# Optimization experiments

Measured on AMD Instinct MI355X. Metric: run time of the kernel, lower is better.

Reference implementation:

```python
import jax, jax.numpy as jnp
import numpy as np

N_NODES = 100000
N_EDGES = 1600000
HID = 128


def setup_inputs() -> dict:
    key = jax.random.key(0)
    ks = jax.random.split(key, 16)

    def w(k, fan_in, fan_out, scale=None):
        s = scale if scale is not None else 1.0 / np.sqrt(fan_in)
        return (jax.random.normal(k, (fan_in, fan_out), jnp.float32) * s)

    inp = {
        "h": jax.random.normal(ks[0], (N_NODES, HID), jnp.float32),
        "edge_index": jax.random.randint(ks[1], (2, N_EDGES), 0, N_NODES, jnp.int64),
        "x": jax.random.normal(ks[2], (N_NODES, 3), jnp.float32),
        "v": jax.random.normal(ks[3], (N_NODES, 3), jnp.float32),
        # edge_mlp: Linear(257,128) -> ReLU -> Linear(128,128) -> ReLU
        "we1": w(ks[4], 2 * HID + 1, HID), "be1": jnp.zeros((HID,), jnp.float32),
        "we2": w(ks[5], HID, HID), "be2": jnp.zeros((HID,), jnp.float32),
        # node_mlp: Linear(384,128) -> ReLU -> Linear(128,128)
        "wn1": w(ks[6], 3 * HID, HID), "bn1": jnp.zeros((HID,), jnp.float32),
        "wn2": w(ks[7], HID, HID), "bn2": jnp.zeros((HID,), jnp.float32),
        # coord_mlp_vel: Linear(128,128) -> ReLU -> Linear(128,1)
        "wv1": w(ks[8], HID, HID), "bv1": jnp.zeros((HID,), jnp.float32),
        "wv2": w(ks[9], HID, 1), "bv2": jnp.zeros((1,), jnp.float32),
        # coord_mlp: Linear(128,128) -> ReLU -> Linear(128,1, bias=False, xavier gain 0.001)
        "wc1": w(ks[10], HID, HID), "bc1": jnp.zeros((HID,), jnp.float32),
        "wc2": w(ks[11], HID, 1, scale=0.001),
    }
    return inp


def reference(h, edge_index, x, v, we1, be1, we2, be2, wn1, bn1, wn2, bn2,
              wv1, bv1, wv2, bv2, wc1, bc1, wc2):
    n = h.shape[0]
    row, col = edge_index[0], edge_index[1]

    # coord2radial
    coord_diff = x[row] - x[col]                                  # [M, 3]
    radial = jnp.sum(coord_diff * coord_diff, axis=1, keepdims=True)  # [M, 1]

    # edge_model (no attention, no edge_attr)
    e_in = jnp.concatenate([h[row], h[col], radial], axis=1)      # [M, 257]
    edge_feat = jax.nn.relu(jax.nn.relu(e_in @ we1 + be1) @ we2 + be2)  # [M, 128]

    # coord_model: per-edge scalar gate, clamp, segment-mean over row
    gate = jax.nn.relu(edge_feat @ wc1 + bc1) @ wc2               # [M, 1]
    trans = jnp.clip(coord_diff * gate, -100.0, 100.0)            # [M, 3]
    num = jax.ops.segment_sum(trans, row, num_segments=n)         # [N, 3]
    cnt = jax.ops.segment_sum(jnp.ones_like(trans), row, num_segments=n)
    f = (num / jnp.maximum(cnt, 1.0)) * 1.0                       # coords_weight = 1.0

    # update: v' = gate(h) * v + f ; x' = x + v'
    vel_gate = jax.nn.relu(h @ wv1 + bv1) @ wv2 + bv2             # [N, 1]
    v_new = vel_gate * v + f
    x_new = x + v_new

    # node_model with others=h: cat[h, h, segment_sum(edge_feat)]
    agg = jax.ops.segment_sum(edge_feat, row, num_segments=n)     # [N, 128]
    n_in = jnp.concatenate([h, h, agg], axis=1)                   # [N, 384]
    h_new = h + (jax.nn.relu(n_in @ wn1 + bn1) @ wn2 + bn2)       # recurrent residual

    return h_new, x_new, v_new
```

## Files before the change

### kernel.cpp

```cpp
#include <hip/hip_runtime.h>
#include <hip/hip_bf16.h>
#include <stdint.h>

typedef __bf16 bf16_t;
typedef __bf16 bf16x8 __attribute__((ext_vector_type(8)));
typedef float f32x4 __attribute__((ext_vector_type(4)));

#define HID 128

__device__ __forceinline__ bf16_t* swz(bf16_t* base, int row, int rowBytes, int byteInRow) {
    return (bf16_t*)((char*)base + row * rowBytes + (byteInRow ^ ((row & 7) << 4)));
}
__device__ __forceinline__ const bf16_t* swzc(const bf16_t* base, int row, int rowBytes, int byteInRow) {
    return (const bf16_t*)((const char*)base + row * rowBytes + (byteInRow ^ ((row & 7) << 4)));
}

__device__ __forceinline__ bf16x8 pack8(float4 a, float4 b) {
    bf16x8 r;
    r[0] = (bf16_t)a.x; r[1] = (bf16_t)a.y; r[2] = (bf16_t)a.z; r[3] = (bf16_t)a.w;
    r[4] = (bf16_t)b.x; r[5] = (bf16_t)b.y; r[6] = (bf16_t)b.z; r[7] = (bf16_t)b.w;
    return r;
}

__device__ __forceinline__ bool is_i64(const int* ei) {
    return ((ei[1] | ei[3] | ei[5] | ei[7]) == 0);
}
__device__ __forceinline__ int eidx(const int* __restrict__ ei, int i, bool i64) {
    return i64 ? ei[2 * i] : ei[i];
}

__global__ void prep_kernel(const float* __restrict__ we1, const float* __restrict__ we2,
                            const float* __restrict__ wc1, const float* __restrict__ wn1,
                            const float* __restrict__ wn2, const float* __restrict__ wv1,
                            bf16_t* w1t, float* w1last, bf16_t* w2t, bf16_t* wc1t,
                            bf16_t* wn1t, bf16_t* wn2t, bf16_t* wv1t) {
    int idx = blockIdx.x * 256 + threadIdx.x;
    if (idx < 32768) { int j = idx >> 8, k = idx & 255; w1t[idx] = (bf16_t)we1[k * 128 + j]; return; }
    idx -= 32768;
    if (idx < 128) { w1last[idx] = we1[256 * 128 + idx]; return; }
    idx -= 128;
    if (idx < 16384) { int j = idx >> 7, k = idx & 127; w2t[idx] = (bf16_t)we2[k * 128 + j]; return; }
    idx -= 16384;
    if (idx < 16384) { int j = idx >> 7, k = idx & 127; wc1t[idx] = (bf16_t)wc1[k * 128 + j]; return; }
    idx -= 16384;
    if (idx < 32768) {
        int j = idx >> 8, k = idx & 255;
        float val = (k < 128) ? (wn1[k * 128 + j] + wn1[(k + 128) * 128 + j])
                              : wn1[(k + 128) * 128 + j];
        wn1t[idx] = (bf16_t)val; return;
    }
    idx -= 32768;
    if (idx < 16384) { int j = idx >> 7, k = idx & 127; wn2t[idx] = (bf16_t)wn2[k * 128 + j]; return; }
    idx -= 16384;
    if (idx < 16384) { int j = idx >> 7, k = idx & 127; wv1t[idx] = (bf16_t)wv1[k * 128 + j]; return; }
}

__global__ __launch_bounds__(512, 2) void edge_kernel(
    const float* __restrict__ h, const int* __restrict__ ei, const float* __restrict__ x,
    const float* __restrict__ be1, const float* __restrict__ be2,
    const float* __restrict__ bc1, const float* __restrict__ wc2,
    const bf16_t* __restrict__ w1t, const float* __restrict__ w1last,
    const bf16_t* __restrict__ w2t, const bf16_t* __restrict__ wc1t,
    float* __restrict__ agg, float* __restrict__ num, float* __restrict__ cnt,
    int M, int N) {
    __shared__ bf16_t lw1[128 * 256];
    __shared__ bf16_t lw2[128 * 128];
    __shared__ bf16_t lbuf[8][2][16 * 128];

    const int tid = threadIdx.x;
    for (int c = tid; c < 4096; c += 512) {
        int row = c >> 5, cin = c & 31;
        float4 d4 = ((const float4*)w1t)[c];
        *(float4*)swz(lw1, row, 512, cin * 16) = d4;
    }
    for (int c = tid; c < 2048; c += 512) {
        int row = c >> 4, cin = c & 15;
        float4 d4 = ((const float4*)w2t)[c];
        *(float4*)swz(lw2, row, 256, cin * 16) = d4;
    }
    __syncthreads();

    const bool i64 = is_i64(ei);
    const int wave = tid >> 6, lane = tid & 63;
    const int l15 = lane & 15, l4 = lane >> 4;
    bf16_t* b0 = lbuf[wave][0];
    bf16_t* b1 = lbuf[wave][1];
    const int wid = blockIdx.x * 8 + wave;
    const int stride = gridDim.x * 8;
    const int ntiles = M >> 4;

    for (int t = wid; t < ntiles; t += stride) {
        const int e0 = t << 4;
        const int s = lane >> 2, p = lane & 3;
        const int er = eidx(ei, e0 + s, i64);
        const int ec = eidx(ei, M + e0 + s, i64);
        const float* hr = h + (size_t)er * HID + p * 32;
        const float* hc = h + (size_t)ec * HID + p * 32;
#pragma unroll
        for (int c2 = 0; c2 < 4; c2++) {
            float4 a = *(const float4*)(hr + c2 * 8);
            float4 b = *(const float4*)(hr + c2 * 8 + 4);
            *(bf16x8*)swz(b0, s, 256, (p * 4 + c2) * 16) = pack8(a, b);
        }
#pragma unroll
        for (int c2 = 0; c2 < 4; c2++) {
            float4 a = *(const float4*)(hc + c2 * 8);
            float4 b = *(const float4*)(hc + c2 * 8 + 4);
            *(bf16x8*)swz(b1, s, 256, (p * 4 + c2) * 16) = pack8(a, b);
        }
        float d0 = x[er * 3 + 0] - x[ec * 3 + 0];
        float d1 = x[er * 3 + 1] - x[ec * 3 + 1];
        float d2 = x[er * 3 + 2] - x[ec * 3 + 2];
        float radial = d0 * d0 + d1 * d1 + d2 * d2;
        __builtin_amdgcn_wave_barrier();

        float rad4[4], dx4[4], dy4[4], dz4[4];
#pragma unroll
        for (int r = 0; r < 4; r++) {
            int src = (l4 * 4 + r) * 4;
            rad4[r] = __shfl(radial, src, 64);
            dx4[r] = __shfl(d0, src, 64);
            dy4[r] = __shfl(d1, src, 64);
            dz4[r] = __shfl(d2, src, 64);
        }

        f32x4 acc[8];
#pragma unroll
        for (int n = 0; n < 8; n++) {
            int j = n * 16 + l15;
            float bb = be1[j], wl = w1last[j];
#pragma unroll
            for (int r = 0; r < 4; r++) acc[n][r] = bb + rad4[r] * wl;
        }
#pragma unroll
        for (int kk = 0; kk < 8; kk++) {
            const bf16_t* ab = (kk < 4) ? b0 : b1;
            bf16x8 af = *(const bf16x8*)swzc(ab, l15, 256, (kk & 3) * 64 + l4 * 16);
#pragma unroll
            for (int n = 0; n < 8; n++) {
                bf16x8 bf = *(const bf16x8*)swzc(lw1, n * 16 + l15, 512, kk * 64 + l4 * 16);
                acc[n] = __builtin_amdgcn_mfma_f32_16x16x32_bf16(af, bf, acc[n], 0, 0, 0);
            }
        }
#pragma unroll
        for (int n = 0; n < 8; n++) {
#pragma unroll
            for (int r = 0; r < 4; r++) {
                int rw = l4 * 4 + r;
                *swz(b0, rw, 256, (n * 16 + l15) * 2) = (bf16_t)fmaxf(acc[n][r], 0.f);
            }
        }
        __builtin_amdgcn_wave_barrier();

        f32x4 acc2[8];
#pragma unroll
        for (int n = 0; n < 8; n++) {
            float bb = be2[n * 16 + l15];
#pragma unroll
            for (int r = 0; r < 4; r++) acc2[n][r] = bb;
        }
#pragma unroll
        for (int kk = 0; kk < 4; kk++) {
            bf16x8 af = *(const bf16x8*)swzc(b0, l15, 256, kk * 64 + l4 * 16);
#pragma unroll
            for (int n = 0; n < 8; n++) {
                bf16x8 bf = *(const bf16x8*)swzc(lw2, n * 16 + l15, 256, kk * 64 + l4 * 16);
                acc2[n] = __builtin_amdgcn_mfma_f32_16x16x32_bf16(af, bf, acc2[n], 0, 0, 0);
            }
        }
        float ef[8][4];
#pragma unroll
        for (int n = 0; n < 8; n++) {
#pragma unroll
            for (int r = 0; r < 4; r++) {
                float v_ = fmaxf(acc2[n][r], 0.f);
                ef[n][r] = v_;
                int rw = l4 * 4 + r;
                *swz(b1, rw, 256, (n * 16 + l15) * 2) = (bf16_t)v_;
            }
        }
        __builtin_amdgcn_wave_barrier();

        f32x4 acc3[8];
#pragma unroll
        for (int n = 0; n < 8; n++) {
            float bb = bc1[n * 16 + l15];
#pragma unroll
            for (int r = 0; r < 4; r++) acc3[n][r] = bb;
        }
#pragma unroll
        for (int kk = 0; kk < 4; kk++) {
            bf16x8 af = *(const bf16x8*)swzc(b1, l15, 256, kk * 64 + l4 * 16);
#pragma unroll
            for (int n = 0; n < 8; n++) {
                bf16x8 bf = *(const bf16x8*)(wc1t + (n * 16 + l15) * 128 + kk * 32 + l4 * 8);
                acc3[n] = __builtin_amdgcn_mfma_f32_16x16x32_bf16(af, bf, acc3[n], 0, 0, 0);
            }
        }
        float pr[4] = {0.f, 0.f, 0.f, 0.f};
#pragma unroll
        for (int n = 0; n < 8; n++) {
            float w = wc2[n * 16 + l15];
#pragma unroll
            for (int r = 0; r < 4; r++) pr[r] += fmaxf(acc3[n][r], 0.f) * w;
        }
#pragma unroll
        for (int m = 1; m < 16; m <<= 1) {
#pragma unroll
            for (int r = 0; r < 4; r++) pr[r] += __shfl_xor(pr[r], m, 16);
        }

        if (l15 == 0) {
#pragma unroll
            for (int r = 0; r < 4; r++) {
                int e = e0 + l4 * 4 + r;
                int re = eidx(ei, e, i64);
                float g = pr[r];
                float t0 = fminf(fmaxf(dx4[r] * g, -100.f), 100.f);
                float t1 = fminf(fmaxf(dy4[r] * g, -100.f), 100.f);
                float t2 = fminf(fmaxf(dz4[r] * g, -100.f), 100.f);
                atomicAdd(num + (size_t)re * 3 + 0, t0);
                atomicAdd(num + (size_t)re * 3 + 1, t1);
                atomicAdd(num + (size_t)re * 3 + 2, t2);
                atomicAdd(cnt + re, 1.0f);
            }
        }
#pragma unroll
        for (int r = 0; r < 4; r++) {
            int e = e0 + l4 * 4 + r;
            int re = eidx(ei, e, i64);
            float* basep = agg + (size_t)re * HID + l15;
#pragma unroll
            for (int n = 0; n < 8; n++) atomicAdd(basep + n * 16, ef[n][r]);
        }
    }
}

__global__ __launch_bounds__(256, 1) void node_kernel(
    const float* __restrict__ h, const float* __restrict__ x, const float* __restrict__ v,
    const float* __restrict__ bn1, const float* __restrict__ bn2,
    const float* __restrict__ bv1, const float* __restrict__ bv2,
    const float* __restrict__ wv2,
    const bf16_t* __restrict__ wn1t, const bf16_t* __restrict__ wn2t,
    const bf16_t* __restrict__ wv1t,
    const float* __restrict__ num, const float* __restrict__ cnt,
    float* __restrict__ out_h, float* __restrict__ out_x, float* __restrict__ out_v,
    int N) {
    __shared__ bf16_t lw1[128 * 256];
    __shared__ bf16_t lw2[128 * 128];
    __shared__ bf16_t lbuf[4][3][16 * 128];

    const int tid = threadIdx.x;
    for (int c = tid; c < 4096; c += 256) {
        int row = c >> 5, cin = c & 31;
        *(float4*)swz(lw1, row, 512, cin * 16) = ((const float4*)wn1t)[c];
    }
    for (int c = tid; c < 2048; c += 256) {
        int row = c >> 4, cin = c & 15;
        *(float4*)swz(lw2, row, 256, cin * 16) = ((const float4*)wn2t)[c];
    }
    __syncthreads();

    const int wave = tid >> 6, lane = tid & 63;
    const int l15 = lane & 15, l4 = lane >> 4;
    bf16_t* b0 = lbuf[wave][0];
    bf16_t* b1 = lbuf[wave][1];
    bf16_t* b2 = lbuf[wave][2];
    const int wid = blockIdx.x * 4 + wave;
    const int stride = gridDim.x * 4;
    const int nt = N >> 4;

    for (int t = wid; t < nt; t += stride) {
        const int m0 = t << 4;
        const int s = lane >> 2, p = lane & 3;
        const float* hp = h + (size_t)(m0 + s) * HID + p * 32;
        const float* ap = out_h + (size_t)(m0 + s) * HID + p * 32;
#pragma unroll
        for (int c2 = 0; c2 < 4; c2++) {
            float4 a = *(const float4*)(hp + c2 * 8);
            float4 b = *(const float4*)(hp + c2 * 8 + 4);
            *(bf16x8*)swz(b0, s, 256, (p * 4 + c2) * 16) = pack8(a, b);
        }
#pragma unroll
        for (int c2 = 0; c2 < 4; c2++) {
            float fa[8];
            *(float4*)fa = *(const float4*)(ap + c2 * 8);
            *(float4*)(fa + 4) = *(const float4*)(ap + c2 * 8 + 4);
            bf16x8 hi8, lo8;
#pragma unroll
            for (int i = 0; i < 8; i++) {
                bf16_t hi = (bf16_t)fa[i];
                hi8[i] = hi;
                lo8[i] = (bf16_t)(fa[i] - (float)hi);
            }
            *(bf16x8*)swz(b1, s, 256, (p * 4 + c2) * 16) = hi8;
            *(bf16x8*)swz(b2, s, 256, (p * 4 + c2) * 16) = lo8;
        }
        __builtin_amdgcn_wave_barrier();

        f32x4 av[8];
#pragma unroll
        for (int n = 0; n < 8; n++) {
            float bb = bv1[n * 16 + l15];
#pragma unroll
            for (int r = 0; r < 4; r++) av[n][r] = bb;
        }
#pragma unroll
        for (int kk = 0; kk < 4; kk++) {
            bf16x8 af = *(const bf16x8*)swzc(b0, l15, 256, kk * 64 + l4 * 16);
#pragma unroll
            for (int n = 0; n < 8; n++) {
                bf16x8 bf = *(const bf16x8*)(wv1t + (n * 16 + l15) * 128 + kk * 32 + l4 * 8);
                av[n] = __builtin_amdgcn_mfma_f32_16x16x32_bf16(af, bf, av[n], 0, 0, 0);
            }
        }
        float pv[4] = {0.f, 0.f, 0.f, 0.f};
#pragma unroll
        for (int n = 0; n < 8; n++) {
            float w = wv2[n * 16 + l15];
#pragma unroll
            for (int r = 0; r < 4; r++) pv[r] += fmaxf(av[n][r], 0.f) * w;
        }
#pragma unroll
        for (int m = 1; m < 16; m <<= 1) {
#pragma unroll
            for (int r = 0; r < 4; r++) pv[r] += __shfl_xor(pv[r], m, 16);
        }
        float bv2v = bv2[0];
        if (l15 == 0) {
#pragma unroll
            for (int r = 0; r < 4; r++) {
                int m = m0 + l4 * 4 + r;
                float vg = pv[r] + bv2v;
                float c = cnt[m];
                float inv = 1.0f / fmaxf(c, 1.0f);
#pragma unroll
                for (int i = 0; i < 3; i++) {
                    float f = num[(size_t)m * 3 + i] * inv;
                    float vn = vg * v[(size_t)m * 3 + i] + f;
                    out_v[(size_t)m * 3 + i] = vn;
                    out_x[(size_t)m * 3 + i] = x[(size_t)m * 3 + i] + vn;
                }
            }
        }

        f32x4 a1[8];
#pragma unroll
        for (int n = 0; n < 8; n++) {
            float bb = bn1[n * 16 + l15];
#pragma unroll
            for (int r = 0; r < 4; r++) a1[n][r] = bb;
        }
#pragma unroll
        for (int kk = 0; kk < 12; kk++) {
            const bf16_t* ab = (kk < 4) ? b0 : ((kk < 8) ? b1 : b2);
            bf16x8 af = *(const bf16x8*)swzc(ab, l15, 256, (kk & 3) * 64 + l4 * 16);
            int kb = (kk < 8) ? kk : (kk - 4);
#pragma unroll
            for (int n = 0; n < 8; n++) {
                bf16x8 bf = *(const bf16x8*)swzc(lw1, n * 16 + l15, 512, kb * 64 + l4 * 16);
                a1[n] = __builtin_amdgcn_mfma_f32_16x16x32_bf16(af, bf, a1[n], 0, 0, 0);
            }
        }
#pragma unroll
        for (int n = 0; n < 8; n++) {
#pragma unroll
            for (int r = 0; r < 4; r++) {
                int rw = l4 * 4 + r;
                *swz(b0, rw, 256, (n * 16 + l15) * 2) = (bf16_t)fmaxf(a1[n][r], 0.f);
            }
        }
        __builtin_amdgcn_wave_barrier();

        f32x4 a2[8];
#pragma unroll
        for (int n = 0; n < 8; n++) {
            float bb = bn2[n * 16 + l15];
#pragma unroll
            for (int r = 0; r < 4; r++) a2[n][r] = bb;
        }
#pragma unroll
        for (int kk = 0; kk < 4; kk++) {
            bf16x8 af = *(const bf16x8*)swzc(b0, l15, 256, kk * 64 + l4 * 16);
#pragma unroll
            for (int n = 0; n < 8; n++) {
                bf16x8 bf = *(const bf16x8*)swzc(lw2, n * 16 + l15, 256, kk * 64 + l4 * 16);
                a2[n] = __builtin_amdgcn_mfma_f32_16x16x32_bf16(af, bf, a2[n], 0, 0, 0);
            }
        }
#pragma unroll
        for (int n = 0; n < 8; n++) {
            int j = n * 16 + l15;
#pragma unroll
            for (int r = 0; r < 4; r++) {
                int m = m0 + l4 * 4 + r;
                out_h[(size_t)m * HID + j] = h[(size_t)m * HID + j] + a2[n][r];
            }
        }
    }
}

extern "C" void kernel_launch(void* const* d_in, const int* in_sizes, int n_in,
                              void* d_out, int out_size, void* d_ws, size_t ws_size,
                              hipStream_t stream) {
    const float* h   = (const float*)d_in[0];
    const int*   ei  = (const int*)d_in[1];
    const float* x   = (const float*)d_in[2];
    const float* v   = (const float*)d_in[3];
    const float* we1 = (const float*)d_in[4];
    const float* be1 = (const float*)d_in[5];
    const float* we2 = (const float*)d_in[6];
    const float* be2 = (const float*)d_in[7];
    const float* wn1 = (const float*)d_in[8];
    const float* bn1 = (const float*)d_in[9];
    const float* wn2 = (const float*)d_in[10];
    const float* bn2 = (const float*)d_in[11];
    const float* wv1 = (const float*)d_in[12];
    const float* bv1 = (const float*)d_in[13];
    const float* wv2 = (const float*)d_in[14];
    const float* bv2 = (const float*)d_in[15];
    const float* wc1 = (const float*)d_in[16];
    const float* bc1 = (const float*)d_in[17];
    const float* wc2 = (const float*)d_in[18];

    const int N = in_sizes[0] / HID;
    const int M = in_sizes[1] / 2;

    float* out_h = (float*)d_out;
    float* out_x = out_h + (size_t)N * HID;
    float* out_v = out_x + (size_t)N * 3;

    char* ws = (char*)d_ws;
    bf16_t* w1t    = (bf16_t*)(ws + 0);
    float*  w1last = (float*)(ws + 65536);
    bf16_t* w2t    = (bf16_t*)(ws + 66048);
    bf16_t* wc1t   = (bf16_t*)(ws + 98816);
    bf16_t* wn1t   = (bf16_t*)(ws + 131584);
    bf16_t* wn2t   = (bf16_t*)(ws + 197120);
    bf16_t* wv1t   = (bf16_t*)(ws + 229888);
    float*  num    = (float*)(ws + 262656);
    float*  cnt    = (float*)(ws + 262656 + (size_t)N * 3 * 4);

    hipMemsetAsync(out_h, 0, (size_t)N * HID * sizeof(float), stream);
    hipMemsetAsync(ws + 262656, 0, (size_t)N * 4 * 4, stream);

    prep_kernel<<<513, 256, 0, stream>>>(we1, we2, wc1, wn1, wn2, wv1,
                                         w1t, w1last, w2t, wc1t, wn1t, wn2t, wv1t);
    edge_kernel<<<256, 512, 0, stream>>>(h, ei, x, be1, be2, bc1, wc2,
                                         w1t, w1last, w2t, wc1t,
                                         out_h, num, cnt, M, N);
    node_kernel<<<256, 256, 0, stream>>>(h, x, v, bn1, bn2, bv1, bv2, wv2,
                                         wn1t, wn2t, wv1t, num, cnt,
                                         out_h, out_x, out_v, N);
}
```

Measured before the change: 1.463 ms.

## Sort edges by destination row via counting sort and pre-reduce scatter atomics

```diff
diff --git a/kernel.cpp b/kernel.cpp
--- a/kernel.cpp
+++ b/kernel.cpp
@@ -55,13 +55,86 @@
     if (idx < 16384) { int j = idx >> 7, k = idx & 127; wv1t[idx] = (bf16_t)wv1[k * 128 + j]; return; }
 }
 
+__global__ void hist_kernel(const int* __restrict__ ei, int* __restrict__ hist, int M) {
+    const bool i64 = is_i64(ei);
+    int e = blockIdx.x * 256 + threadIdx.x;
+    if (e < M) atomicAdd(&hist[eidx(ei, e, i64)], 1);
+}
+
+#define NCHUNK 128
+__global__ void scanA_kernel(const int* __restrict__ hist, int* __restrict__ chunk_sums,
+                             int N, int CHUNK) {
+    __shared__ int red[256];
+    int b = blockIdx.x, tid = threadIdx.x;
+    int lo = b * CHUNK, hi = min(N, lo + CHUNK);
+    int s = 0;
+    for (int i = lo + tid; i < hi; i += 256) s += hist[i];
+    red[tid] = s; __syncthreads();
+    for (int ofs = 128; ofs > 0; ofs >>= 1) {
+        if (tid < ofs) red[tid] += red[tid + ofs];
+        __syncthreads();
+    }
+    if (tid == 0) chunk_sums[b] = red[0];
+}
+
+__global__ void scanB_kernel(const int* __restrict__ chunk_sums, int* __restrict__ chunk_base,
+                             int* __restrict__ off, int N, int M) {
+    __shared__ int s[NCHUNK];
+    int tid = threadIdx.x;
+    if (tid < NCHUNK) s[tid] = chunk_sums[tid];
+    __syncthreads();
+    if (tid == 0) {
+        int run = 0;
+        for (int i = 0; i < NCHUNK; i++) { int v = s[i]; s[i] = run; run += v; }
+        off[N] = M;
+    }
+    __syncthreads();
+    if (tid < NCHUNK) chunk_base[tid] = s[tid];
+}
+
+__global__ void scanC_kernel(const int* __restrict__ hist, const int* __restrict__ chunk_base,
+                             int* __restrict__ off, int* __restrict__ cursor, int N, int CHUNK) {
+    __shared__ int sd[256];
+    int b = blockIdx.x, tid = threadIdx.x;
+    int carry = chunk_base[b];
+    for (int base = 0; base < CHUNK; base += 256) {
+        int li = base + tid;
+        int i = b * CHUNK + li;
+        int v = (li < CHUNK && i < N) ? hist[i] : 0;
+        sd[tid] = v; __syncthreads();
+        for (int ofs = 1; ofs < 256; ofs <<= 1) {
+            int t = (tid >= ofs) ? sd[tid - ofs] : 0;
+            __syncthreads();
+            sd[tid] += t;
+            __syncthreads();
+        }
+        int excl = sd[tid] - v;
+        if (li < CHUNK && i < N) { off[i] = carry + excl; cursor[i] = carry + excl; }
+        carry += sd[255];
+        __syncthreads();
+    }
+}
+
+__global__ void scatter_kernel(const int* __restrict__ ei, int* __restrict__ cursor,
+                               int* __restrict__ sorted_eid, int* __restrict__ sorted_row, int M) {
+    const bool i64 = is_i64(ei);
+    int e = blockIdx.x * 256 + threadIdx.x;
+    if (e < M) {
+        int r = eidx(ei, e, i64);
+        int p = atomicAdd(&cursor[r], 1);
+        sorted_eid[p] = e;
+        sorted_row[p] = r;
+    }
+}
+
 __global__ __launch_bounds__(512, 2) void edge_kernel(
     const float* __restrict__ h, const int* __restrict__ ei, const float* __restrict__ x,
     const float* __restrict__ be1, const float* __restrict__ be2,
     const float* __restrict__ bc1, const float* __restrict__ wc2,
     const bf16_t* __restrict__ w1t, const float* __restrict__ w1last,
     const bf16_t* __restrict__ w2t, const bf16_t* __restrict__ wc1t,
-    float* __restrict__ agg, float* __restrict__ num, float* __restrict__ cnt,
+    const int* __restrict__ sorted_eid, const int* __restrict__ sorted_row,
+    float* __restrict__ agg, float* __restrict__ num,
     int M, int N) {
     __shared__ bf16_t lw1[128 * 256];
     __shared__ bf16_t lw2[128 * 128];
@@ -92,8 +165,9 @@
     for (int t = wid; t < ntiles; t += stride) {
         const int e0 = t << 4;
         const int s = lane >> 2, p = lane & 3;
-        const int er = eidx(ei, e0 + s, i64);
-        const int ec = eidx(ei, M + e0 + s, i64);
+        const int er = sorted_row[e0 + s];
+        const int eid = sorted_eid[e0 + s];
+        const int ec = eidx(ei, M + eid, i64);
         const float* hr = h + (size_t)er * HID + p * 32;
         const float* hc = h + (size_t)ec * HID + p * 32;
 #pragma unroll
@@ -114,15 +188,9 @@
         float radial = d0 * d0 + d1 * d1 + d2 * d2;
         __builtin_amdgcn_wave_barrier();
 
-        float rad4[4], dx4[4], dy4[4], dz4[4];
-#pragma unroll
-        for (int r = 0; r < 4; r++) {
-            int src = (l4 * 4 + r) * 4;
-            rad4[r] = __shfl(radial, src, 64);
-            dx4[r] = __shfl(d0, src, 64);
-            dy4[r] = __shfl(d1, src, 64);
-            dz4[r] = __shfl(d2, src, 64);
-        }
+        float rad4[4];
+#pragma unroll
+        for (int r = 0; r < 4; r++) rad4[r] = __shfl(radial, (l4 * 4 + r) * 4, 64);
 
         f32x4 acc[8];
 #pragma unroll
@@ -168,13 +236,11 @@
                 acc2[n] = __builtin_amdgcn_mfma_f32_16x16x32_bf16(af, bf, acc2[n], 0, 0, 0);
             }
         }
-        float ef[8][4];
 #pragma unroll
         for (int n = 0; n < 8; n++) {
 #pragma unroll
             for (int r = 0; r < 4; r++) {
                 float v_ = fmaxf(acc2[n][r], 0.f);
-                ef[n][r] = v_;
                 int rw = l4 * 4 + r;
                 *swz(b1, rw, 256, (n * 16 + l15) * 2) = (bf16_t)v_;
             }
@@ -210,29 +276,40 @@
             for (int r = 0; r < 4; r++) pr[r] += __shfl_xor(pr[r], m, 16);
         }
 
-        if (l15 == 0) {
-#pragma unroll
-            for (int r = 0; r < 4; r++) {
-                int e = e0 + l4 * 4 + r;
-                int re = eidx(ei, e, i64);
-                float g = pr[r];
-                float t0 = fminf(fmaxf(dx4[r] * g, -100.f), 100.f);
-                float t1 = fminf(fmaxf(dy4[r] * g, -100.f), 100.f);
-                float t2 = fminf(fmaxf(dz4[r] * g, -100.f), 100.f);
-                atomicAdd(num + (size_t)re * 3 + 0, t0);
-                atomicAdd(num + (size_t)re * 3 + 1, t1);
-                atomicAdd(num + (size_t)re * 3 + 2, t2);
-                atomicAdd(cnt + re, 1.0f);
-            }
-        }
-#pragma unroll
-        for (int r = 0; r < 4; r++) {
-            int e = e0 + l4 * 4 + r;
-            int re = eidx(ei, e, i64);
-            float* basep = agg + (size_t)re * HID + l15;
-#pragma unroll
-            for (int n = 0; n < 8; n++) atomicAdd(basep + n * 16, ef[n][r]);
-        }
+        {
+            int s3 = s & 3;
+            float g = (s3 == 0) ? pr[0] : ((s3 == 1) ? pr[1] : ((s3 == 2) ? pr[2] : pr[3]));
+            if ((lane & 3) == 0) {
+                float t0 = fminf(fmaxf(d0 * g, -100.f), 100.f);
+                float t1 = fminf(fmaxf(d1 * g, -100.f), 100.f);
+                float t2 = fminf(fmaxf(d2 * g, -100.f), 100.f);
+                atomicAdd(num + (size_t)er * 3 + 0, t0);
+                atomicAdd(num + (size_t)er * 3 + 1, t1);
+                atomicAdd(num + (size_t)er * 3 + 2, t2);
+            }
+        }
+
+        int er16[16];
+#pragma unroll
+        for (int rw = 0; rw < 16; rw++) er16[rw] = __shfl(er, rw * 4, 64);
+
+        const int c0 = lane, c1 = lane + 64;
+        float s0 = 0.f, s1 = 0.f;
+        int prev = er16[0];
+#pragma unroll
+        for (int rw = 0; rw < 16; rw++) {
+            if (rw > 0 && er16[rw] != prev) {
+                atomicAdd(agg + (size_t)prev * HID + c0, s0);
+                atomicAdd(agg + (size_t)prev * HID + c1, s1);
+                s0 = 0.f; s1 = 0.f;
+                prev = er16[rw];
+            }
+            s0 += (float)*swzc(b1, rw, 256, c0 * 2);
+            s1 += (float)*swzc(b1, rw, 256, c1 * 2);
+        }
+        atomicAdd(agg + (size_t)prev * HID + c0, s0);
+        atomicAdd(agg + (size_t)prev * HID + c1, s1);
+        __builtin_amdgcn_wave_barrier();
     }
 }
 
@@ -243,7 +320,7 @@
     const float* __restrict__ wv2,
     const bf16_t* __restrict__ wn1t, const bf16_t* __restrict__ wn2t,
     const bf16_t* __restrict__ wv1t,
-    const float* __restrict__ num, const float* __restrict__ cnt,
+    const float* __restrict__ num, const int* __restrict__ off,
     float* __restrict__ out_h, float* __restrict__ out_x, float* __restrict__ out_v,
     int N) {
     __shared__ bf16_t lw1[128 * 256];
@@ -332,7 +409,7 @@
             for (int r = 0; r < 4; r++) {
                 int m = m0 + l4 * 4 + r;
                 float vg = pv[r] + bv2v;
-                float c = cnt[m];
+                float c = (float)(off[m + 1] - off[m]);
                 float inv = 1.0f / fmaxf(c, 1.0f);
 #pragma unroll
                 for (int i = 0; i < 3; i++) {
@@ -431,25 +508,43 @@
     float* out_v = out_x + (size_t)N * 3;
 
     char* ws = (char*)d_ws;
-    bf16_t* w1t    = (bf16_t*)(ws + 0);
-    float*  w1last = (float*)(ws + 65536);
-    bf16_t* w2t    = (bf16_t*)(ws + 66048);
-    bf16_t* wc1t   = (bf16_t*)(ws + 98816);
-    bf16_t* wn1t   = (bf16_t*)(ws + 131584);
-    bf16_t* wn2t   = (bf16_t*)(ws + 197120);
-    bf16_t* wv1t   = (bf16_t*)(ws + 229888);
-    float*  num    = (float*)(ws + 262656);
-    float*  cnt    = (float*)(ws + 262656 + (size_t)N * 3 * 4);
+    auto align256 = [](size_t v) { return (v + 255) & ~(size_t)255; };
+    size_t o = 0;
+    bf16_t* w1t    = (bf16_t*)(ws + o); o += 65536;
+    float*  w1last = (float*)(ws + o);  o += 512;
+    bf16_t* w2t    = (bf16_t*)(ws + o); o += 32768;
+    bf16_t* wc1t   = (bf16_t*)(ws + o); o += 32768;
+    bf16_t* wn1t   = (bf16_t*)(ws + o); o += 65536;
+    bf16_t* wn2t   = (bf16_t*)(ws + o); o += 32768;
+    bf16_t* wv1t   = (bf16_t*)(ws + o); o += 32768;
+    float*  num    = (float*)(ws + o);        o = align256(o + (size_t)N * 12);
+    int*    hist   = (int*)(ws + o);          o = align256(o + (size_t)N * 4);
+    int*    off    = (int*)(ws + o);          o = align256(o + (size_t)(N + 1) * 4);
+    int*    cursor = (int*)(ws + o);          o = align256(o + (size_t)N * 4);
+    int*    chunk_sums = (int*)(ws + o);      o = align256(o + NCHUNK * 4);
+    int*    chunk_base = (int*)(ws + o);      o = align256(o + NCHUNK * 4);
+    int*    sorted_eid = (int*)(ws + o);      o = align256(o + (size_t)M * 4);
+    int*    sorted_row = (int*)(ws + o);      o = align256(o + (size_t)M * 4);
+
+    const int CHUNK = (N + NCHUNK - 1) / NCHUNK;
 
     hipMemsetAsync(out_h, 0, (size_t)N * HID * sizeof(float), stream);
-    hipMemsetAsync(ws + 262656, 0, (size_t)N * 4 * 4, stream);
+    hipMemsetAsync(num, 0, (size_t)N * 12, stream);
+    hipMemsetAsync(hist, 0, (size_t)N * 4, stream);
 
     prep_kernel<<<513, 256, 0, stream>>>(we1, we2, wc1, wn1, wn2, wv1,
                                          w1t, w1last, w2t, wc1t, wn1t, wn2t, wv1t);
+    hist_kernel<<<(M + 255) / 256, 256, 0, stream>>>(ei, hist, M);
+    scanA_kernel<<<NCHUNK, 256, 0, stream>>>(hist, chunk_sums, N, CHUNK);
+    scanB_kernel<<<1, 256, 0, stream>>>(chunk_sums, chunk_base, off, N, M);
+    scanC_kernel<<<NCHUNK, 256, 0, stream>>>(hist, chunk_base, off, cursor, N, CHUNK);
+    scatter_kernel<<<(M + 255) / 256, 256, 0, stream>>>(ei, cursor, sorted_eid, sorted_row, M);
+
     edge_kernel<<<256, 512, 0, stream>>>(h, ei, x, be1, be2, bc1, wc2,
                                          w1t, w1last, w2t, wc1t,
-                                         out_h, num, cnt, M, N);
+                                         sorted_eid, sorted_row,
+                                         out_h, num, M, N);
     node_kernel<<<256, 256, 0, stream>>>(h, x, v, bn1, bn2, bv1, bv2, wv2,
-                                         wn1t, wn2t, wv1t, num, cnt,
+                                         wn1t, wn2t, wv1t, num, off,
                                          out_h, out_x, out_v, N);
 }
```

After: 1.568 ms. 1.07x slower.
